# Kernel tuning notes

Measured on AMD Instinct MI355X. Metric: run time of the kernel, lower is better.

## Reference

```python
import jax, jax.numpy as jnp
import numpy as np

B, S, D, H, F = 16, 512, 768, 12, 3072
E = 4      # unique sequence-level experts
M = 4      # inner SwitchFeedForward experts
SW = 128   # switch encoder dim
EPS = 1e-12


def setup_inputs() -> dict:
    key = jax.random.key(0)
    ks = iter(jax.random.split(key, 64))
    def p(shape):
        return jax.random.normal(next(ks), shape, jnp.float32) * 0.02
    inp = {}
    inp['hidden_states'] = jax.random.normal(next(ks), (B, S, D), jnp.float32)
    inp['attention_mask'] = jnp.zeros((B, S), jnp.float32)
    inp['cluster_list'] = jnp.zeros((B,), jnp.int32)
    # router
    inp['sw_enc_w'] = p((D, SW)); inp['sw_enc_b'] = jnp.zeros((SW,), jnp.float32)
    inp['sw_w'] = p((SW, E));     inp['sw_b'] = jnp.zeros((E,), jnp.float32)
    # common attention
    for n in ('q', 'k', 'v', 'o'):
        inp['ca_w' + n] = p((D, D)); inp['ca_b' + n] = jnp.zeros((D,), jnp.float32)
    # unique attentions (stacked over E experts)
    for n in ('q', 'k', 'v', 'o'):
        inp['ua_w' + n] = p((E, D, D)); inp['ua_b' + n] = jnp.zeros((E, D), jnp.float32)
    # common FFN (plain GELU MLP)
    inp['cf_w1'] = p((D, F)); inp['cf_b1'] = jnp.zeros((F,), jnp.float32)
    inp['cf_w2'] = p((F, D)); inp['cf_b2'] = jnp.zeros((D,), jnp.float32)
    # unique FFNs: each is a top-1 SwitchFeedForward with M inner experts
    inp['uf_sw_w'] = p((E, D, M)); inp['uf_sw_b'] = jnp.zeros((E, M), jnp.float32)
    inp['uf_w1'] = p((E, M, D, F)); inp['uf_b1'] = jnp.zeros((E, M, F), jnp.float32)
    inp['uf_w2'] = p((E, M, F, D)); inp['uf_b2'] = jnp.zeros((E, M, D), jnp.float32)
    # output LayerNorm
    inp['ln_g'] = jnp.ones((D,), jnp.float32); inp['ln_b'] = jnp.zeros((D,), jnp.float32)
    return inp


def _attn(x, mask, wq, bq, wk, bk, wv, bv, wo, bo):
    b, s, d = x.shape
    dh = d // H
    q = (x @ wq + bq).reshape(b, s, H, dh)
    k = (x @ wk + bk).reshape(b, s, H, dh)
    v = (x @ wv + bv).reshape(b, s, H, dh)
    sc = jnp.einsum('bqhd,bkhd->bhqk', q, k) / jnp.sqrt(jnp.float32(dh))
    sc = sc + mask[:, None, None, :]
    pr = jax.nn.softmax(sc, axis=-1)
    o = jnp.einsum('bhqk,bkhd->bqhd', pr, v).reshape(b, s, d)
    return o @ wo + bo


def _switch_ffn(x, sww, swb, w1, b1, w2, b2):
    # top-1 token routing over M inner experts, output scaled by route_prob_max
    rp = jax.nn.softmax(x @ sww + swb, axis=-1)            # [b,s,M]
    gate = jax.nn.one_hot(jnp.argmax(rp, -1), M) * jnp.max(rp, -1, keepdims=True)
    h = jax.nn.gelu(jnp.einsum('bsd,mdf->bsmf', x, w1) + b1, approximate=False)
    y = jnp.einsum('bsmf,mfd->bsmd', h, w2) + b2
    return jnp.einsum('bsm,bsmd->bsd', gate, y)


def _forward(hidden_states, attention_mask, sw_enc_w, sw_enc_b, sw_w, sw_b,
             ca_wq, ca_bq, ca_wk, ca_bk, ca_wv, ca_bv, ca_wo, ca_bo,
             ua_wq, ua_bq, ua_wk, ua_bk, ua_wv, ua_bv, ua_wo, ua_bo,
             cf_w1, cf_b1, cf_w2, cf_b2,
             uf_sw_w, uf_sw_b, uf_w1, uf_b1, uf_w2, uf_b2, ln_g, ln_b):
    # sequence-level router: softmax over pooled hidden states, top-1 expert
    pooled = hidden_states.mean(axis=1)                    # [B,D]
    rp = jax.nn.softmax((pooled @ sw_enc_w + sw_enc_b) @ sw_w + sw_b, axis=-1)
    pm = jnp.max(rp, axis=-1)                              # [B]
    sel = jax.nn.one_hot(jnp.argmax(rp, axis=-1), E)       # [B,E]

    common_attn = _attn(hidden_states, attention_mask,
                        ca_wq, ca_bq, ca_wk, ca_bk, ca_wv, ca_bv, ca_wo, ca_bo)
    unique_attn = jnp.zeros_like(hidden_states)
    for i in range(E):
        oi = _attn(hidden_states, attention_mask,
                   ua_wq[i], ua_bq[i], ua_wk[i], ua_bk[i],
                   ua_wv[i], ua_bv[i], ua_wo[i], ua_bo[i])
        unique_attn = unique_attn + sel[:, i, None, None] * oi
    unique_attn = unique_attn * pm[:, None, None]          # scale by route prob
    att_output = common_attn + unique_attn

    unique_ffn = jnp.zeros_like(hidden_states)
    for i in range(E):
        yi = _switch_ffn(att_output, uf_sw_w[i], uf_sw_b[i],
                         uf_w1[i], uf_b1[i], uf_w2[i], uf_b2[i])
        unique_ffn = unique_ffn + sel[:, i, None, None] * yi
    common_ffn = jax.nn.gelu(att_output @ cf_w1 + cf_b1, approximate=False) @ cf_w2 + cf_b2
    ffn_output = common_ffn + unique_ffn                   # dropout is identity (eval)

    x = att_output + ffn_output
    mu = x.mean(-1, keepdims=True)
    var = jnp.mean((x - mu) ** 2, -1, keepdims=True)
    return (x - mu) / jnp.sqrt(var + EPS) * ln_g + ln_b


def reference(hidden_states, attention_mask, cluster_list, sw_enc_w, sw_enc_b, sw_w, sw_b,
              ca_wq, ca_bq, ca_wk, ca_bk, ca_wv, ca_bv, ca_wo, ca_bo,
              ua_wq, ua_bq, ua_wk, ua_bk, ua_wv, ua_bv, ua_wo, ua_bo,
              cf_w1, cf_b1, cf_w2, cf_b2,
              uf_sw_w, uf_sw_b, uf_w1, uf_b1, uf_w2, uf_b2, ln_g, ln_b):
    # cluster_list is only used in the warm-up branch; warm_up_step=0 -> ignored
    return _forward(hidden_states, attention_mask, sw_enc_w, sw_enc_b, sw_w, sw_b,
                    ca_wq, ca_bq, ca_wk, ca_bk, ca_wv, ca_bv, ca_wo, ca_bo,
                    ua_wq, ua_bq, ua_wk, ua_bk, ua_wv, ua_bv, ua_wo, ua_bo,
                    cf_w1, cf_b1, cf_w2, cf_b2,
                    uf_sw_w, uf_sw_b, uf_w1, uf_b1, uf_w2, uf_b2, ln_g, ln_b)
```

## Files before the change

### kernel.cpp

```cpp
#include <hip/hip_runtime.h>
#include <cstdint>
#include <cstddef>

#define Bq  16
#define Sq  512
#define Dq  768
#define Hq  12
#define DHq 64
#define Fq  3072
#define SWq 128
#define NTq 8192

typedef float        f32x4  __attribute__((ext_vector_type(4)));
typedef float        f32x16 __attribute__((ext_vector_type(16)));
typedef unsigned int u32x4  __attribute__((ext_vector_type(4)));
typedef __bf16       bf16x8 __attribute__((ext_vector_type(8)));
typedef _Float16     f16x8  __attribute__((ext_vector_type(8)));
typedef _Float16     f16x4  __attribute__((ext_vector_type(4)));
typedef _Float16     f16x2  __attribute__((ext_vector_type(2)));
typedef int          i32x2  __attribute__((ext_vector_type(2)));

__device__ __forceinline__ unsigned short f2bf(float f){
  unsigned int u = __builtin_bit_cast(unsigned int, f);
  u = (u + 0x7fffu + ((u >> 16) & 1u)) >> 16;
  return (unsigned short)u;
}
__device__ __forceinline__ unsigned int pk2(float a, float b){
  return (unsigned int)f2bf(a) | ((unsigned int)f2bf(b) << 16);
}
__device__ __forceinline__ i32x2 pl32swap(unsigned int a, unsigned int b){
  return __builtin_amdgcn_permlane32_swap((int)a, (int)b, false, false);
}
__device__ __forceinline__ f16x2 cvt_pk(float a, float b){
  return __builtin_bit_cast(f16x2, __builtin_amdgcn_cvt_pkrtz(a, b));
}

__device__ __forceinline__ void swz2d(int &bx, int &by){
  const int gx = gridDim.x, gy = gridDim.y;
  const int nb = gx * gy;
  const int bid = blockIdx.y * gx + blockIdx.x;
  if (((nb & 7) == 0) && ((gy & 7) == 0)){
    const int chunk = nb >> 3;
    const int lb = (bid & 7) * chunk + (bid >> 3);
    const int bw = gx << 3;
    const int band = lb / bw;
    const int wn = lb - band * bw;
    bx = wn >> 3;
    by = (band << 3) + (wn & 7);
  } else {
    bx = blockIdx.x; by = blockIdx.y;
  }
}

__global__ void pooled_partial_k(const float* __restrict__ x, float* __restrict__ part){
  const int b = blockIdx.x, dc = blockIdx.y, z = blockIdx.z;
  const int d = dc*256 + threadIdx.x;
  const float* p = x + (size_t)b*Sq*Dq + (size_t)z*128*Dq + d;
  float s = 0.f;
  #pragma unroll 4
  for (int i = 0; i < 128; i++) s += p[(size_t)i*Dq];
  part[((size_t)z*Bq + b)*Dq + d] = s;
}

__global__ void router_seq_k(const float* __restrict__ part,
    const float* __restrict__ ew, const float* __restrict__ eb,
    const float* __restrict__ sw, const float* __restrict__ sb,
    int* __restrict__ sel, float* __restrict__ pm)
{
  const int b = blockIdx.x, j = threadIdx.x;
  __shared__ float h[SWq];
  __shared__ float pl[Dq];
  #pragma unroll
  for (int i = 0; i < 6; i++){
    int d = j + i*128;
    float s = part[(size_t)(0*Bq+b)*Dq + d] + part[(size_t)(1*Bq+b)*Dq + d]
            + part[(size_t)(2*Bq+b)*Dq + d] + part[(size_t)(3*Bq+b)*Dq + d];
    pl[d] = s * (1.0f/512.0f);
  }
  __syncthreads();
  float a = eb[j];
  for (int d = 0; d < Dq; d++) a += pl[d] * ew[d*SWq + j];
  h[j] = a;
  __syncthreads();
  if (j == 0){
    float lg[4];
    for (int e = 0; e < 4; e++){
      float t = sb[e];
      for (int k = 0; k < SWq; k++) t += h[k] * sw[k*4 + e];
      lg[e] = t;
    }
    float mx = fmaxf(fmaxf(lg[0],lg[1]), fmaxf(lg[2],lg[3]));
    float p[4], ssum = 0.f;
    for (int e = 0; e < 4; e++){ p[e] = expf(lg[e]-mx); ssum += p[e]; }
    int am = 0; float bv = p[0];
    for (int e = 1; e < 4; e++) if (p[e] > bv){ bv = p[e]; am = e; }
    sel[b] = am; pm[b] = bv/ssum;
  }
}

__global__ void split_f16_k(const float* __restrict__ x, _Float16* __restrict__ hh,
                            _Float16* __restrict__ ll, int n4){
  const int i = blockIdx.x*256 + threadIdx.x;
  if (i >= n4) return;
  f32x4 v = ((const f32x4*)x)[i];
  f16x4 vh, vl;
  #pragma unroll
  for (int j = 0; j < 4; j++){
    float s = v[j] * 1024.0f;
    _Float16 a = (_Float16)s;
    vh[j] = a;
    vl[j] = (_Float16)(s - (float)a);
  }
  ((f16x4*)hh)[i] = vh;
  ((f16x4*)ll)[i] = vl;
}

__global__ void transpose_f16s_k(const float* __restrict__ src,
    _Float16* __restrict__ dH, _Float16* __restrict__ dL,
    int K, int N, long srcStride, long dstStride, int rowOff)
{
  __shared__ float t[64][65];
  const int tid = threadIdx.x;
  const size_t so = (size_t)blockIdx.z * srcStride;
  const size_t dof = (size_t)blockIdx.z * dstStride;
  const int k0 = blockIdx.y * 64, n0 = blockIdx.x * 64;
  const int r = tid >> 2, c0 = (tid & 3) * 16;
  const float* sp = src + so + (size_t)(k0 + r) * N + n0 + c0;
  #pragma unroll
  for (int cc = 0; cc < 16; cc += 4){
    f32x4 v = *(const f32x4*)(sp + cc);
    t[r][c0+cc] = v[0]; t[r][c0+cc+1] = v[1]; t[r][c0+cc+2] = v[2]; t[r][c0+cc+3] = v[3];
  }
  __syncthreads();
  _Float16* ph = dH + dof + (size_t)(rowOff + n0 + r) * K + k0 + c0;
  _Float16* pl = dL + dof + (size_t)(rowOff + n0 + r) * K + k0 + c0;
  #pragma unroll
  for (int cc = 0; cc < 16; cc += 4){
    f16x4 vh, vl;
    #pragma unroll
    for (int j = 0; j < 4; j++){
      float s = t[c0+cc+j][r] * 1024.0f;
      _Float16 a = (_Float16)s;
      vh[j] = a; vl[j] = (_Float16)(s - (float)a);
    }
    *(f16x4*)(ph + cc) = vh;
    *(f16x4*)(pl + cc) = vl;
  }
}

__global__ void concat_bias3_k(const float* __restrict__ bq, const float* __restrict__ bk,
    const float* __restrict__ bv, float* __restrict__ dst, int srcStride)
{
  const int e = blockIdx.y;
  const int i = blockIdx.x*256 + threadIdx.x;
  dst[(size_t)e*2304 + i]        = bq[(size_t)e*srcStride + i];
  dst[(size_t)e*2304 + 768 + i]  = bk[(size_t)e*srcStride + i];
  dst[(size_t)e*2304 + 1536 + i] = bv[(size_t)e*srcStride + i];
}

template<int BMODE, int OMODE>
__global__ __launch_bounds__(256,2) void gemm_f16s_k(
    const _Float16* __restrict__ AH, const _Float16* __restrict__ AL,
    const _Float16* __restrict__ BH, const _Float16* __restrict__ BL,
    const float* __restrict__ bias, float* __restrict__ C,
    _Float16* __restrict__ Ch, _Float16* __restrict__ Cl,
    int N, int K, long estride, int bias_stride,
    const int* __restrict__ sel, const float* __restrict__ pm)
{
  __shared__ _Float16 AsH[128][40];
  __shared__ _Float16 AsL[128][40];
  __shared__ _Float16 BsH[128][40];
  __shared__ _Float16 BsL[128][40];
  const int tid = threadIdx.x;
  const int lane = tid & 63, wave = tid >> 6;
  const int wm = wave >> 1, wn = wave & 1;
  int bx, by; swz2d(bx, by);
  const int row0 = by * 128, col0 = bx * 128;
  const _Float16* bh = BH; const _Float16* bl = BL; const float* bp = bias;
  float cs = 1.0f;
  if constexpr (BMODE == 1){
    const int e = sel[row0 >> 9];
    bh += (size_t)e * estride; bl += (size_t)e * estride;
    bp += (size_t)e * bias_stride;
  }
  if constexpr (OMODE == 1) cs = pm[row0 >> 9];

  const int sr = tid >> 1, sk = (tid & 1) * 16;
  const _Float16* ahp = AH + (size_t)(row0 + sr) * K + sk;
  const _Float16* alp = AL + (size_t)(row0 + sr) * K + sk;
  const _Float16* bhp = bh + (size_t)(col0 + sr) * K + sk;
  const _Float16* blp = bl + (size_t)(col0 + sr) * K + sk;

  f32x4 acc[4][4];
  #pragma unroll
  for (int mi=0;mi<4;mi++)
    #pragma unroll
    for (int ni=0;ni<4;ni++) acc[mi][ni] = (f32x4){0.f,0.f,0.f,0.f};

  for (int k0 = 0; k0 < K; k0 += 32){
    u32x4 vah0 = *(const u32x4*)(ahp + k0);
    u32x4 vah1 = *(const u32x4*)(ahp + k0 + 8);
    u32x4 val0 = *(const u32x4*)(alp + k0);
    u32x4 val1 = *(const u32x4*)(alp + k0 + 8);
    u32x4 vbh0 = *(const u32x4*)(bhp + k0);
    u32x4 vbh1 = *(const u32x4*)(bhp + k0 + 8);
    u32x4 vbl0 = *(const u32x4*)(blp + k0);
    u32x4 vbl1 = *(const u32x4*)(blp + k0 + 8);
    __syncthreads();
    *(u32x4*)&AsH[sr][sk]   = vah0; *(u32x4*)&AsH[sr][sk+8] = vah1;
    *(u32x4*)&AsL[sr][sk]   = val0; *(u32x4*)&AsL[sr][sk+8] = val1;
    *(u32x4*)&BsH[sr][sk]   = vbh0; *(u32x4*)&BsH[sr][sk+8] = vbh1;
    *(u32x4*)&BsL[sr][sk]   = vbl0; *(u32x4*)&BsL[sr][sk+8] = vbl1;
    __syncthreads();
    f16x8 fah[4], fal[4], fbh[4], fbl[4];
    #pragma unroll
    for (int mi=0;mi<4;mi++){
      const int r = wm*64 + mi*16 + (lane&15), c = 8*(lane>>4);
      fah[mi] = __builtin_bit_cast(f16x8, *(const u32x4*)&AsH[r][c]);
      fal[mi] = __builtin_bit_cast(f16x8, *(const u32x4*)&AsL[r][c]);
    }
    #pragma unroll
    for (int ni=0;ni<4;ni++){
      const int r = wn*64 + ni*16 + (lane&15), c = 8*(lane>>4);
      fbh[ni] = __builtin_bit_cast(f16x8, *(const u32x4*)&BsH[r][c]);
      fbl[ni] = __builtin_bit_cast(f16x8, *(const u32x4*)&BsL[r][c]);
    }
    #pragma unroll
    for (int mi=0;mi<4;mi++)
      #pragma unroll
      for (int ni=0;ni<4;ni++){
        acc[mi][ni] = __builtin_amdgcn_mfma_f32_16x16x32_f16(fah[mi], fbh[ni], acc[mi][ni], 0, 0, 0);
        acc[mi][ni] = __builtin_amdgcn_mfma_f32_16x16x32_f16(fah[mi], fbl[ni], acc[mi][ni], 0, 0, 0);
        acc[mi][ni] = __builtin_amdgcn_mfma_f32_16x16x32_f16(fal[mi], fbh[ni], acc[mi][ni], 0, 0, 0);
      }
  }

  const float INV = 1.0f/1048576.0f;
  const int erow = 4*(lane >> 4);
  const int ecol = lane & 15;
  #pragma unroll
  for (int mi=0;mi<4;mi++)
    #pragma unroll
    for (int ni=0;ni<4;ni++){
      const int c = col0 + wn*64 + ni*16 + ecol;
      const float bb = bp[c];
      #pragma unroll
      for (int r=0;r<4;r++){
        const int R = row0 + wm*64 + mi*16 + erow + r;
        const float v = acc[mi][ni][r]*INV + bb;
        if constexpr (OMODE == 0){
          C[(size_t)R*N + c] = v;
        } else if constexpr (OMODE == 1){
          C[(size_t)R*N + c] += cs*v;
        } else {
          const float vs = v * 1024.0f;
          const _Float16 hi = (_Float16)vs;
          Ch[(size_t)R*N + c] = hi;
          Cl[(size_t)R*N + c] = (_Float16)(vs - (float)hi);
        }
      }
    }
}

__global__ __launch_bounds__(256,2) void attn_mfma_k(
    const _Float16* __restrict__ qkvH, const _Float16* __restrict__ qkvL,
    const float* __restrict__ mask,
    _Float16* __restrict__ ctxH, _Float16* __restrict__ ctxL)
{
  __shared__ _Float16 Kh[64][72], Kl[64][72];
  __shared__ _Float16 Vh[64][72], Vl[64][72];
  __shared__ float msk[64];
  __shared__ float rsi[4][32];
  const int qb = blockIdx.x, h = blockIdx.y, b = blockIdx.z;
  const int tid = threadIdx.x;
  const int l = tid & 63, w = tid >> 6;
  const int l31 = l & 31, g5 = l >> 5;
  const float SC = 1.0f/8388608.0f;

  u32x4 qfh[4], qfl[4];
  {
    const size_t qoff = (size_t)(b*Sq + qb*128 + w*32 + l31) * 2304 + h*DHq + g5*8;
    #pragma unroll
    for (int c = 0; c < 4; c++){
      qfh[c] = *(const u32x4*)(qkvH + qoff + c*16);
      qfl[c] = *(const u32x4*)(qkvL + qoff + c*16);
    }
  }
  f32x16 oacc[2];
  #pragma unroll
  for (int nt = 0; nt < 2; nt++)
    #pragma unroll
    for (int i = 0; i < 16; i++) oacc[nt][i] = 0.f;
  float rsl = 0.f;
  const float* mrow = mask + b*Sq;

  for (int kt = 0; kt < 8; kt++){
    __syncthreads();
    {
      const size_t krow = (size_t)(b*Sq + kt*64 + l) * 2304 + 768 + h*DHq;
      #pragma unroll
      for (int i = 0; i < 2; i++){
        const int ch = w + i*4;
        *(u32x4*)&Kh[l][ch*8] = *(const u32x4*)(qkvH + krow + ch*8);
        *(u32x4*)&Kl[l][ch*8] = *(const u32x4*)(qkvL + krow + ch*8);
      }
      const size_t vrow = krow + 768 + w*16;
      f16x8 v0 = __builtin_bit_cast(f16x8, *(const u32x4*)(qkvH + vrow));
      f16x8 v1 = __builtin_bit_cast(f16x8, *(const u32x4*)(qkvH + vrow + 8));
      f16x8 u0 = __builtin_bit_cast(f16x8, *(const u32x4*)(qkvL + vrow));
      f16x8 u1 = __builtin_bit_cast(f16x8, *(const u32x4*)(qkvL + vrow + 8));
      #pragma unroll
      for (int i = 0; i < 8; i++){
        Vh[w*16 + i][l] = v0[i]; Vh[w*16 + 8 + i][l] = v1[i];
        Vl[w*16 + i][l] = u0[i]; Vl[w*16 + 8 + i][l] = u1[i];
      }
      if (tid < 64) msk[tid] = mrow[kt*64 + tid] + 6.9314718055994531f;
    }
    __syncthreads();

    f32x16 sacc[2];
    #pragma unroll
    for (int mt = 0; mt < 2; mt++)
      #pragma unroll
      for (int i = 0; i < 16; i++) sacc[mt][i] = 0.f;
    #pragma unroll
    for (int mt = 0; mt < 2; mt++){
      #pragma unroll
      for (int c = 0; c < 4; c++){
        f16x8 kh = __builtin_bit_cast(f16x8, *(const u32x4*)&Kh[mt*32 + l31][c*16 + g5*8]);
        f16x8 kl = __builtin_bit_cast(f16x8, *(const u32x4*)&Kl[mt*32 + l31][c*16 + g5*8]);
        f16x8 qh = __builtin_bit_cast(f16x8, qfh[c]);
        f16x8 ql = __builtin_bit_cast(f16x8, qfl[c]);
        sacc[mt] = __builtin_amdgcn_mfma_f32_32x32x16_f16(kh, qh, sacc[mt], 0, 0, 0);
        sacc[mt] = __builtin_amdgcn_mfma_f32_32x32x16_f16(kh, ql, sacc[mt], 0, 0, 0);
        sacc[mt] = __builtin_amdgcn_mfma_f32_32x32x16_f16(kl, qh, sacc[mt], 0, 0, 0);
      }
    }

    unsigned int hP[2][4][2], lP[2][4][2];
    #pragma unroll
    for (int mt = 0; mt < 2; mt++){
      #pragma unroll
      for (int m = 0; m < 4; m++){
        f32x4 mk = *(const f32x4*)&msk[mt*32 + m*8 + g5*4];
        float p0 = __expf(fmaf(sacc[mt][4*m+0], SC, mk[0]));
        float p1 = __expf(fmaf(sacc[mt][4*m+1], SC, mk[1]));
        float p2 = __expf(fmaf(sacc[mt][4*m+2], SC, mk[2]));
        float p3 = __expf(fmaf(sacc[mt][4*m+3], SC, mk[3]));
        rsl += (p0 + p1) + (p2 + p3);
        f16x2 h0 = cvt_pk(p0, p1);
        f16x2 h1 = cvt_pk(p2, p3);
        f16x2 e0, e1;
        e0[0] = (_Float16)(p0 - (float)h0[0]); e0[1] = (_Float16)(p1 - (float)h0[1]);
        e1[0] = (_Float16)(p2 - (float)h1[0]); e1[1] = (_Float16)(p3 - (float)h1[1]);
        hP[mt][m][0] = __builtin_bit_cast(unsigned int, h0);
        hP[mt][m][1] = __builtin_bit_cast(unsigned int, h1);
        lP[mt][m][0] = __builtin_bit_cast(unsigned int, e0);
        lP[mt][m][1] = __builtin_bit_cast(unsigned int, e1);
      }
    }

    #pragma unroll
    for (int mt = 0; mt < 2; mt++){
      #pragma unroll
      for (int cc = 0; cc < 2; cc++){
        i32x2 sh0 = pl32swap(hP[mt][2*cc][0], hP[mt][2*cc+1][0]);
        i32x2 sh1 = pl32swap(hP[mt][2*cc][1], hP[mt][2*cc+1][1]);
        i32x2 sl0 = pl32swap(lP[mt][2*cc][0], lP[mt][2*cc+1][0]);
        i32x2 sl1 = pl32swap(lP[mt][2*cc][1], lP[mt][2*cc+1][1]);
        u32x4 pah = (u32x4){(unsigned)sh0[0], (unsigned)sh1[0], (unsigned)sh0[1], (unsigned)sh1[1]};
        u32x4 pal = (u32x4){(unsigned)sl0[0], (unsigned)sl1[0], (unsigned)sl0[1], (unsigned)sl1[1]};
        f16x8 ph = __builtin_bit_cast(f16x8, pah);
        f16x8 pe = __builtin_bit_cast(f16x8, pal);
        const int kof = (mt*2 + cc)*16 + g5*8;
        #pragma unroll
        for (int nt = 0; nt < 2; nt++){
          f16x8 vh = __builtin_bit_cast(f16x8, *(const u32x4*)&Vh[nt*32 + l31][kof]);
          f16x8 vl = __builtin_bit_cast(f16x8, *(const u32x4*)&Vl[nt*32 + l31][kof]);
          oacc[nt] = __builtin_amdgcn_mfma_f32_32x32x16_f16(ph, vh, oacc[nt], 0, 0, 0);
          oacc[nt] = __builtin_amdgcn_mfma_f32_32x32x16_f16(ph, vl, oacc[nt], 0, 0, 0);
          oacc[nt] = __builtin_amdgcn_mfma_f32_32x32x16_f16(pe, vh, oacc[nt], 0, 0, 0);
        }
      }
    }
  }

  {
    unsigned int rb = __builtin_bit_cast(unsigned int, rsl);
    i32x2 sw = pl32swap(rb, rb);
    float partner = __builtin_bit_cast(float, (l >= 32) ? sw[0] : sw[1]);
    float tot = rsl + partner;
    if (l < 32) rsi[w][l31] = 1.0f / tot;
  }
  __syncthreads();

  const size_t obase = (size_t)(b*Sq + qb*128 + w*32);
  #pragma unroll
  for (int nt = 0; nt < 2; nt++){
    const int col = h*DHq + nt*32 + l31;
    #pragma unroll
    for (int r = 0; r < 16; r++){
      const int q = (r&3) + 8*(r>>2) + 4*g5;
      const float v = oacc[nt][r] * rsi[w][q];
      const _Float16 hi = (_Float16)v;
      const size_t off = (obase + q)*Dq + col;
      ctxH[off] = hi;
      ctxL[off] = (_Float16)(v - (float)hi);
    }
  }
}

__global__ void transpose_bf16_k(const float* __restrict__ src, unsigned short* __restrict__ dst,
                                 int K, int N)
{
  __shared__ float t[64][65];
  const int tid = threadIdx.x;
  const size_t mo = (size_t)blockIdx.z * K * N;
  const int k0 = blockIdx.y * 64, n0 = blockIdx.x * 64;
  const int r = tid >> 2, c0 = (tid & 3) * 16;
  const float* sp = src + mo + (size_t)(k0 + r) * N + n0 + c0;
  #pragma unroll
  for (int cc = 0; cc < 16; cc += 4){
    f32x4 v = *(const f32x4*)(sp + cc);
    t[r][c0+cc] = v[0]; t[r][c0+cc+1] = v[1]; t[r][c0+cc+2] = v[2]; t[r][c0+cc+3] = v[3];
  }
  __syncthreads();
  unsigned short* dp = dst + mo + (size_t)(n0 + r) * K + k0 + c0;
  u32x4 h0, h1v;
  #pragma unroll
  for (int i = 0; i < 4; i++) h0[i]  = pk2(t[c0+2*i  ][r], t[c0+2*i+1][r]);
  #pragma unroll
  for (int i = 0; i < 4; i++) h1v[i] = pk2(t[c0+8+2*i][r], t[c0+9+2*i][r]);
  *(u32x4*)(dp)     = h0;
  *(u32x4*)(dp + 8) = h1v;
}

template<int AMODE, int OMODE, bool GELU_, bool GROUPED>
__global__ __launch_bounds__(256,2) void gemm_bf16_k(
    const void* __restrict__ Av, const unsigned short* __restrict__ BT,
    const float* __restrict__ bias, float* __restrict__ Cf, unsigned short* __restrict__ Cb,
    int M, int N, int K,
    const int* __restrict__ tile_g, const int* __restrict__ tile_r0,
    const int* __restrict__ grp_off, const int* __restrict__ n_tiles,
    const int* __restrict__ tok_idx, const float* __restrict__ gate_s,
    size_t bstride, int bias_stride)
{
  __shared__ unsigned short As[128][40];
  __shared__ unsigned short Bs[128][40];
  const int tid = threadIdx.x;
  const int lane = tid & 63, wave = tid >> 6;
  const int wm = wave >> 1, wn = wave & 1;
  int col0, row0, gend = 1 << 30, g = 0;
  if constexpr (GROUPED){
    const int t = blockIdx.y;
    if (t >= *n_tiles) return;
    g = tile_g[t];
    row0 = grp_off[g] + tile_r0[t];
    gend = grp_off[g+1];
    col0 = blockIdx.x * 128;
  } else {
    int bx, by; swz2d(bx, by);
    row0 = by * 128;
    col0 = bx * 128;
  }
  const unsigned short* Bp = BT + (size_t)g * bstride;
  const float* bp = bias + (size_t)g * bias_stride;

  const int sr = tid >> 1;
  const int sk = (tid & 1) * 16;
  int arow = row0 + sr;
  if constexpr (GROUPED) arow = (arow < gend - 1) ? arow : (gend - 1);
  if constexpr (AMODE == 1) arow = tok_idx[arow];
  const float*          afp = (const float*)Av          + (size_t)arow * K + sk;
  const unsigned short* abp = (const unsigned short*)Av + (size_t)arow * K + sk;
  const unsigned short* bfp = Bp + (size_t)(col0 + sr) * K + sk;

  f32x4 acc[4][4];
  #pragma unroll
  for (int mi=0;mi<4;mi++)
    #pragma unroll
    for (int ni=0;ni<4;ni++) acc[mi][ni] = (f32x4){0.f,0.f,0.f,0.f};

  for (int k0 = 0; k0 < K; k0 += 32){
    u32x4 bl0 = *(const u32x4*)(bfp + k0);
    u32x4 bl1 = *(const u32x4*)(bfp + k0 + 8);
    u32x4 al0, al1;
    if constexpr (AMODE == 2){
      al0 = *(const u32x4*)(abp + k0);
      al1 = *(const u32x4*)(abp + k0 + 8);
    } else {
      f32x4 f0 = *(const f32x4*)(afp + k0);
      f32x4 f1 = *(const f32x4*)(afp + k0 + 4);
      f32x4 f2 = *(const f32x4*)(afp + k0 + 8);
      f32x4 f3 = *(const f32x4*)(afp + k0 + 12);
      al0[0]=pk2(f0[0],f0[1]); al0[1]=pk2(f0[2],f0[3]); al0[2]=pk2(f1[0],f1[1]); al0[3]=pk2(f1[2],f1[3]);
      al1[0]=pk2(f2[0],f2[1]); al1[1]=pk2(f2[2],f2[3]); al1[2]=pk2(f3[0],f3[1]); al1[3]=pk2(f3[2],f3[3]);
    }
    __syncthreads();
    *(u32x4*)&As[sr][sk]     = al0;
    *(u32x4*)&As[sr][sk + 8] = al1;
    *(u32x4*)&Bs[sr][sk]     = bl0;
    *(u32x4*)&Bs[sr][sk + 8] = bl1;
    __syncthreads();
    bf16x8 af[4], bfr[4];
    #pragma unroll
    for (int mi=0;mi<4;mi++){
      u32x4 t = *(const u32x4*)&As[wm*64 + mi*16 + (lane&15)][8*(lane>>4)];
      af[mi] = __builtin_bit_cast(bf16x8, t);
    }
    #pragma unroll
    for (int ni=0;ni<4;ni++){
      u32x4 t = *(const u32x4*)&Bs[wn*64 + ni*16 + (lane&15)][8*(lane>>4)];
      bfr[ni] = __builtin_bit_cast(bf16x8, t);
    }
    #pragma unroll
    for (int mi=0;mi<4;mi++)
      #pragma unroll
      for (int ni=0;ni<4;ni++)
        acc[mi][ni] = __builtin_amdgcn_mfma_f32_16x16x32_bf16(af[mi], bfr[ni], acc[mi][ni], 0, 0, 0);
  }

  const int erow = 4*(lane >> 4);
  const int ecol = lane & 15;
  #pragma unroll
  for (int mi=0;mi<4;mi++)
    #pragma unroll
    for (int ni=0;ni<4;ni++){
      const int c = col0 + wn*64 + ni*16 + ecol;
      const float bb = bp[c];
      #pragma unroll
      for (int r=0;r<4;r++){
        const int R = row0 + wm*64 + mi*16 + erow + r;
        if (GROUPED && R >= gend) continue;
        float v = acc[mi][ni][r] + bb;
        if (GELU_) v = 0.5f*v*(1.0f + erff(v*0.70710678118654752f));
        if constexpr (OMODE == 0){
          Cb[(size_t)R*N + c] = f2bf(v);
        } else if constexpr (OMODE == 1){
          Cf[(size_t)R*N + c] = v;
        } else {
          const int tok = tok_idx[R];
          const float gt = gate_s[R];
          float* p = Cf + (size_t)tok*N + c;
          *p += gt*v;
        }
      }
    }
}

__global__ void token_router_k(const float* __restrict__ att, const int* __restrict__ sel,
    const float* __restrict__ sww, const float* __restrict__ swb,
    int* __restrict__ grp, float* __restrict__ gate, int* __restrict__ grp_cnt)
{
  const int t = blockIdx.x*4 + (threadIdx.x >> 6);
  const int lane = threadIdx.x & 63;
  const int e = sel[t >> 9];
  const float* x = att + (size_t)t * Dq;
  const float* w = sww + (size_t)e * Dq * 4;
  float a0=0.f, a1=0.f, a2=0.f, a3=0.f;
  #pragma unroll 4
  for (int i = 0; i < 12; i++){
    const int d = lane + i*64;
    const float xv = x[d];
    f32x4 wv = *(const f32x4*)&w[d*4];
    a0 += xv*wv[0]; a1 += xv*wv[1]; a2 += xv*wv[2]; a3 += xv*wv[3];
  }
  #pragma unroll
  for (int off = 32; off; off >>= 1){
    a0 += __shfl_xor(a0, off); a1 += __shfl_xor(a1, off);
    a2 += __shfl_xor(a2, off); a3 += __shfl_xor(a3, off);
  }
  if (lane == 0){
    const float l0 = a0 + swb[e*4+0], l1 = a1 + swb[e*4+1];
    const float l2 = a2 + swb[e*4+2], l3 = a3 + swb[e*4+3];
    const float mx = fmaxf(fmaxf(l0,l1), fmaxf(l2,l3));
    const float p0 = expf(l0-mx), p1 = expf(l1-mx), p2 = expf(l2-mx), p3 = expf(l3-mx);
    const float ssum = p0+p1+p2+p3;
    int am = 0; float bv = p0;
    if (p1 > bv){ bv=p1; am=1; }
    if (p2 > bv){ bv=p2; am=2; }
    if (p3 > bv){ bv=p3; am=3; }
    grp[t] = e*4 + am;
    gate[t] = bv/ssum;
    atomicAdd(&grp_cnt[e*4 + am], 1);
  }
}

__global__ void build_offsets_k(const int* __restrict__ grp_cnt, int* __restrict__ grp_off,
    int* __restrict__ tile_g, int* __restrict__ tile_r0, int* __restrict__ n_tiles)
{
  int off = 0, nt = 0;
  for (int g = 0; g < 16; g++){
    grp_off[g] = off;
    const int c = grp_cnt[g];
    for (int r0 = 0; r0 < c; r0 += 128){ tile_g[nt] = g; tile_r0[nt] = r0; nt++; }
    off += c;
  }
  grp_off[16] = off;
  *n_tiles = nt;
}

__global__ void scatter_k(const int* __restrict__ grp, const float* __restrict__ gate,
    const int* __restrict__ grp_off, int* __restrict__ fill,
    int* __restrict__ tok_idx, float* __restrict__ gate_s)
{
  const int t = blockIdx.x*256 + threadIdx.x;
  const int g = grp[t];
  const int pos = grp_off[g] + atomicAdd(&fill[g], 1);
  tok_idx[pos] = t;
  gate_s[pos] = gate[t];
}

__global__ __launch_bounds__(256) void final_ln_k(const float* __restrict__ att,
    const float* __restrict__ acc, const float* __restrict__ lg,
    const float* __restrict__ lb, float* __restrict__ out)
{
  const int row = blockIdx.x, tid = threadIdx.x;
  const float* a = att + (size_t)row * Dq;
  const float* c = acc + (size_t)row * Dq;
  float x[3];
  #pragma unroll
  for (int i = 0; i < 3; i++) x[i] = a[tid + 256*i] + c[tid + 256*i];
  __shared__ float red[256];
  red[tid] = x[0] + x[1] + x[2];
  __syncthreads();
  for (int st = 128; st; st >>= 1){
    if (tid < st) red[tid] += red[tid + st];
    __syncthreads();
  }
  const float mu = red[0] * (1.0f/768.0f);
  __syncthreads();
  const float d0 = x[0]-mu, d1 = x[1]-mu, d2 = x[2]-mu;
  red[tid] = d0*d0 + d1*d1 + d2*d2;
  __syncthreads();
  for (int st = 128; st; st >>= 1){
    if (tid < st) red[tid] += red[tid + st];
    __syncthreads();
  }
  const float inv = 1.0f/sqrtf(red[0]*(1.0f/768.0f) + 1e-12f);
  #pragma unroll
  for (int i = 0; i < 3; i++){
    const int col = tid + 256*i;
    out[(size_t)row*Dq + col] = (x[i]-mu)*inv*lg[col] + lb[col];
  }
}

extern "C" void kernel_launch(void* const* d_in, const int* in_sizes, int n_in,
                              void* d_out, int out_size, void* d_ws, size_t ws_size,
                              hipStream_t stream)
{
  (void)in_sizes; (void)n_in; (void)out_size; (void)ws_size;
  const float* hs    = (const float*)d_in[0];
  const float* amask = (const float*)d_in[1];
  const float* sw_enc_w = (const float*)d_in[3];
  const float* sw_enc_b = (const float*)d_in[4];
  const float* sw_w  = (const float*)d_in[5];
  const float* sw_b  = (const float*)d_in[6];
  const float* ca_wq = (const float*)d_in[7];
  const float* ca_bq = (const float*)d_in[8];
  const float* ca_wk = (const float*)d_in[9];
  const float* ca_bk = (const float*)d_in[10];
  const float* ca_wv = (const float*)d_in[11];
  const float* ca_bv = (const float*)d_in[12];
  const float* ca_wo = (const float*)d_in[13];
  const float* ca_bo = (const float*)d_in[14];
  const float* ua_wq = (const float*)d_in[15];
  const float* ua_bq = (const float*)d_in[16];
  const float* ua_wk = (const float*)d_in[17];
  const float* ua_bk = (const float*)d_in[18];
  const float* ua_wv = (const float*)d_in[19];
  const float* ua_bv = (const float*)d_in[20];
  const float* ua_wo = (const float*)d_in[21];
  const float* ua_bo = (const float*)d_in[22];
  const float* cf_w1 = (const float*)d_in[23];
  const float* cf_b1 = (const float*)d_in[24];
  const float* cf_w2 = (const float*)d_in[25];
  const float* cf_b2 = (const float*)d_in[26];
  const float* uf_sw_w = (const float*)d_in[27];
  const float* uf_sw_b = (const float*)d_in[28];
  const float* uf_w1 = (const float*)d_in[29];
  const float* uf_b1 = (const float*)d_in[30];
  const float* uf_w2 = (const float*)d_in[31];
  const float* uf_b2 = (const float*)d_in[32];
  const float* ln_g  = (const float*)d_in[33];
  const float* ln_b  = (const float*)d_in[34];
  float* out = (float*)d_out;

  char* W = (char*)d_ws;
  int*   sel     = (int*)(W + 0);
  float* pm      = (float*)(W + 64);
  int*   grp_cnt = (int*)(W + 128);
  int*   fill    = (int*)(W + 192);
  int*   ntile   = (int*)(W + 256);
  int*   grp_off = (int*)(W + 512);
  int*   tile_g  = (int*)(W + 1024);
  int*   tile_r  = (int*)(W + 2048);

  float* att  = (float*)(W + 4096);
  float* facc = (float*)(W + 25169920);
  const size_t X = 50335744;
  _Float16* hsH  = (_Float16*)(W + X);
  _Float16* hsL  = (_Float16*)(W + X + 12582912);
  _Float16* qkvH = (_Float16*)(W + X + 25165824);
  _Float16* qkvL = (_Float16*)(W + X + 62914560);
  _Float16* ctxH = (_Float16*)(W + X + 100663296);
  _Float16* ctxL = (_Float16*)(W + X + 113246208);
  _Float16* wqkv_cH = (_Float16*)(W + X + 125829120);
  _Float16* wqkv_cL = (_Float16*)(W + X + 129368064);
  _Float16* wqkv_uH = (_Float16*)(W + X + 132907008);
  _Float16* wqkv_uL = (_Float16*)(W + X + 147062784);
  _Float16* wo_cH   = (_Float16*)(W + X + 161218560);
  _Float16* wo_cL   = (_Float16*)(W + X + 162398208);
  _Float16* wo_uH   = (_Float16*)(W + X + 163577856);
  _Float16* wo_uL   = (_Float16*)(W + X + 168296448);
  float* qkvb_c = (float*)(W + X + 173015040);
  float* qkvb_u = (float*)(W + X + 173024256);
  float* partb  = (float*)(W + X + 173061120);

  unsigned short* w1T = (unsigned short*)(W + X);
  unsigned short* w2T = (unsigned short*)(W + X + 80216064);
  unsigned short* h1  = (unsigned short*)(W + X + 160432128);
  int*   grp     = (int*)(W + 261099520);
  float* gate    = (float*)(W + 261132288);
  int*   tok_idx = (int*)(W + 261165056);
  float* gate_s  = (float*)(W + 261197824);

  hipMemsetAsync(W, 0, 3072, stream);

  pooled_partial_k<<<dim3(Bq,3,4),256,0,stream>>>(hs, partb);
  router_seq_k<<<Bq,128,0,stream>>>(partb, sw_enc_w, sw_enc_b, sw_w, sw_b, sel, pm);

  split_f16_k<<<6144,256,0,stream>>>(hs, hsH, hsL, NTq*Dq/4);
  transpose_f16s_k<<<dim3(12,12,1),256,0,stream>>>(ca_wq, wqkv_cH, wqkv_cL, Dq, Dq, 0, 0, 0);
  transpose_f16s_k<<<dim3(12,12,1),256,0,stream>>>(ca_wk, wqkv_cH, wqkv_cL, Dq, Dq, 0, 0, 768);
  transpose_f16s_k<<<dim3(12,12,1),256,0,stream>>>(ca_wv, wqkv_cH, wqkv_cL, Dq, Dq, 0, 0, 1536);
  transpose_f16s_k<<<dim3(12,12,4),256,0,stream>>>(ua_wq, wqkv_uH, wqkv_uL, Dq, Dq, (long)Dq*Dq, (long)2304*768, 0);
  transpose_f16s_k<<<dim3(12,12,4),256,0,stream>>>(ua_wk, wqkv_uH, wqkv_uL, Dq, Dq, (long)Dq*Dq, (long)2304*768, 768);
  transpose_f16s_k<<<dim3(12,12,4),256,0,stream>>>(ua_wv, wqkv_uH, wqkv_uL, Dq, Dq, (long)Dq*Dq, (long)2304*768, 1536);
  transpose_f16s_k<<<dim3(12,12,1),256,0,stream>>>(ca_wo, wo_cH, wo_cL, Dq, Dq, 0, 0, 0);
  transpose_f16s_k<<<dim3(12,12,4),256,0,stream>>>(ua_wo, wo_uH, wo_uL, Dq, Dq, (long)Dq*Dq, (long)Dq*Dq, 0);
  concat_bias3_k<<<dim3(3,1),256,0,stream>>>(ca_bq, ca_bk, ca_bv, qkvb_c, 0);
  concat_bias3_k<<<dim3(3,4),256,0,stream>>>(ua_bq, ua_bk, ua_bv, qkvb_u, 768);

  gemm_f16s_k<0,2><<<dim3(18,64),256,0,stream>>>(hsH, hsL, wqkv_cH, wqkv_cL, qkvb_c,
      nullptr, qkvH, qkvL, 2304, Dq, 0, 0, nullptr, nullptr);
  attn_mfma_k<<<dim3(4,Hq,Bq),256,0,stream>>>(qkvH, qkvL, amask, ctxH, ctxL);
  gemm_f16s_k<0,0><<<dim3(6,64),256,0,stream>>>(ctxH, ctxL, wo_cH, wo_cL, ca_bo,
      att, nullptr, nullptr, Dq, Dq, 0, 0, nullptr, nullptr);

  gemm_f16s_k<1,2><<<dim3(18,64),256,0,stream>>>(hsH, hsL, wqkv_uH, wqkv_uL, qkvb_u,
      nullptr, qkvH, qkvL, 2304, Dq, (long)2304*768, 2304, sel, nullptr);
  attn_mfma_k<<<dim3(4,Hq,Bq),256,0,stream>>>(qkvH, qkvL, amask, ctxH, ctxL);
  gemm_f16s_k<1,1><<<dim3(6,64),256,0,stream>>>(ctxH, ctxL, wo_uH, wo_uL, ua_bo,
      att, nullptr, nullptr, Dq, Dq, (long)Dq*Dq, Dq, sel, pm);

  transpose_bf16_k<<<dim3(48,12,1), 256,0,stream>>>(cf_w1, w1T, Dq, Fq);
  transpose_bf16_k<<<dim3(48,12,16),256,0,stream>>>(uf_w1, w1T + 2359296, Dq, Fq);
  transpose_bf16_k<<<dim3(12,48,1), 256,0,stream>>>(cf_w2, w2T, Fq, Dq);
  transpose_bf16_k<<<dim3(12,48,16),256,0,stream>>>(uf_w2, w2T + 2359296, Fq, Dq);

  gemm_bf16_k<0,0,true,false><<<dim3(24,64),256,0,stream>>>((const void*)att, w1T, cf_b1, nullptr, h1,
      NTq, Fq, Dq, nullptr,nullptr,nullptr,nullptr,nullptr,nullptr, (size_t)0, 0);
  gemm_bf16_k<2,1,false,false><<<dim3(6,64),256,0,stream>>>((const void*)h1, w2T, cf_b2, facc, nullptr,
      NTq, Dq, Fq, nullptr,nullptr,nullptr,nullptr,nullptr,nullptr, (size_t)0, 0);

  token_router_k<<<2048,256,0,stream>>>(att, sel, uf_sw_w, uf_sw_b, grp, gate, grp_cnt);
  build_offsets_k<<<1,1,0,stream>>>(grp_cnt, grp_off, tile_g, tile_r, ntile);
  scatter_k<<<32,256,0,stream>>>(grp, gate, grp_off, fill, tok_idx, gate_s);

  gemm_bf16_k<1,0,true,true><<<dim3(24,80),256,0,stream>>>((const void*)att, w1T + 2359296, uf_b1, nullptr, h1,
      NTq, Fq, Dq, tile_g, tile_r, grp_off, ntile, tok_idx, gate_s, (size_t)2359296, Fq);
  gemm_bf16_k<2,2,false,true><<<dim3(6,80),256,0,stream>>>((const void*)h1, w2T + 2359296, uf_b2, facc, nullptr,
      NTq, Dq, Fq, tile_g, tile_r, grp_off, ntile, tok_idx, gate_s, (size_t)2359296, Dq);

  final_ln_k<<<NTq,256,0,stream>>>(att, facc, ln_g, ln_b, out);
}
```

Before: 1.224 ms.

## Use 64-row tiles for down-projection GEMMs and remap grouped tile order

Templates the bf16 GEMM on row-tile height and runs the two F->D down-projection GEMMs (common and grouped expert) with 64-row tiles. This doubles their block count so the small N=768 grids fill more compute units. The grouped kernel also remaps the linear block index with a stride-8 interleave, and build_offsets now emits both 128-row and 64-row tile lists. In exchange, each block reuses fewer B-tile loads per MFMA, and the shared-memory layout shifts.

```diff
diff --git a/kernel.cpp b/kernel.cpp
--- a/kernel.cpp
+++ b/kernel.cpp
@@ -435,49 +435,57 @@
   *(u32x4*)(dp + 8) = h1v;
 }
 
-template<int AMODE, int OMODE, bool GELU_, bool GROUPED>
+template<int MT, int AMODE, int OMODE, bool GELU_, bool GROUPED>
 __global__ __launch_bounds__(256,2) void gemm_bf16_k(
     const void* __restrict__ Av, const unsigned short* __restrict__ BT,
     const float* __restrict__ bias, float* __restrict__ Cf, unsigned short* __restrict__ Cb,
-    int M, int N, int K,
+    int N, int K,
     const int* __restrict__ tile_g, const int* __restrict__ tile_r0,
     const int* __restrict__ grp_off, const int* __restrict__ n_tiles,
     const int* __restrict__ tok_idx, const float* __restrict__ gate_s,
     size_t bstride, int bias_stride)
 {
-  __shared__ unsigned short As[128][40];
+  constexpr int MI = MT / 32;
+  __shared__ unsigned short As[MT][40];
   __shared__ unsigned short Bs[128][40];
   const int tid = threadIdx.x;
   const int lane = tid & 63, wave = tid >> 6;
   const int wm = wave >> 1, wn = wave & 1;
   int col0, row0, gend = 1 << 30, g = 0;
   if constexpr (GROUPED){
-    const int t = blockIdx.y;
+    const int gx = gridDim.x;
+    const int nb = gx * gridDim.y;
+    const int bid = blockIdx.y * gx + blockIdx.x;
+    int lb = bid;
+    if ((nb & 7) == 0) lb = (bid & 7) * (nb >> 3) + (bid >> 3);
+    const int t = lb / gx;
+    col0 = (lb - t * gx) * 128;
     if (t >= *n_tiles) return;
     g = tile_g[t];
     row0 = grp_off[g] + tile_r0[t];
     gend = grp_off[g+1];
-    col0 = blockIdx.x * 128;
   } else {
     int bx, by; swz2d(bx, by);
-    row0 = by * 128;
+    row0 = by * MT;
     col0 = bx * 128;
   }
   const unsigned short* Bp = BT + (size_t)g * bstride;
   const float* bp = bias + (size_t)g * bias_stride;
 
-  const int sr = tid >> 1;
-  const int sk = (tid & 1) * 16;
-  int arow = row0 + sr;
+  const int sa_r = (MT == 128) ? (tid >> 1) : (tid >> 2);
+  const int sa_k = (MT == 128) ? ((tid & 1) * 16) : ((tid & 3) * 8);
+  const int sb_r = tid >> 1;
+  const int sb_k = (tid & 1) * 16;
+  int arow = row0 + sa_r;
   if constexpr (GROUPED) arow = (arow < gend - 1) ? arow : (gend - 1);
   if constexpr (AMODE == 1) arow = tok_idx[arow];
-  const float*          afp = (const float*)Av          + (size_t)arow * K + sk;
-  const unsigned short* abp = (const unsigned short*)Av + (size_t)arow * K + sk;
-  const unsigned short* bfp = Bp + (size_t)(col0 + sr) * K + sk;
-
-  f32x4 acc[4][4];
-  #pragma unroll
-  for (int mi=0;mi<4;mi++)
+  const float*          afp = (const float*)Av          + (size_t)arow * K + sa_k;
+  const unsigned short* abp = (const unsigned short*)Av + (size_t)arow * K + sa_k;
+  const unsigned short* bfp = Bp + (size_t)(col0 + sb_r) * K + sb_k;
+
+  f32x4 acc[MI][4];
+  #pragma unroll
+  for (int mi=0;mi<MI;mi++)
     #pragma unroll
     for (int ni=0;ni<4;ni++) acc[mi][ni] = (f32x4){0.f,0.f,0.f,0.f};
 
@@ -487,25 +495,27 @@
     u32x4 al0, al1;
     if constexpr (AMODE == 2){
       al0 = *(const u32x4*)(abp + k0);
-      al1 = *(const u32x4*)(abp + k0 + 8);
+      if constexpr (MT == 128) al1 = *(const u32x4*)(abp + k0 + 8);
     } else {
       f32x4 f0 = *(const f32x4*)(afp + k0);
       f32x4 f1 = *(const f32x4*)(afp + k0 + 4);
-      f32x4 f2 = *(const f32x4*)(afp + k0 + 8);
-      f32x4 f3 = *(const f32x4*)(afp + k0 + 12);
       al0[0]=pk2(f0[0],f0[1]); al0[1]=pk2(f0[2],f0[3]); al0[2]=pk2(f1[0],f1[1]); al0[3]=pk2(f1[2],f1[3]);
-      al1[0]=pk2(f2[0],f2[1]); al1[1]=pk2(f2[2],f2[3]); al1[2]=pk2(f3[0],f3[1]); al1[3]=pk2(f3[2],f3[3]);
+      if constexpr (MT == 128){
+        f32x4 f2 = *(const f32x4*)(afp + k0 + 8);
+        f32x4 f3 = *(const f32x4*)(afp + k0 + 12);
+        al1[0]=pk2(f2[0],f2[1]); al1[1]=pk2(f2[2],f2[3]); al1[2]=pk2(f3[0],f3[1]); al1[3]=pk2(f3[2],f3[3]);
+      }
     }
     __syncthreads();
-    *(u32x4*)&As[sr][sk]     = al0;
-    *(u32x4*)&As[sr][sk + 8] = al1;
-    *(u32x4*)&Bs[sr][sk]     = bl0;
-    *(u32x4*)&Bs[sr][sk + 8] = bl1;
+    *(u32x4*)&As[sa_r][sa_k] = al0;
+    if constexpr (MT == 128) *(u32x4*)&As[sa_r][sa_k + 8] = al1;
+    *(u32x4*)&Bs[sb_r][sb_k]     = bl0;
+    *(u32x4*)&Bs[sb_r][sb_k + 8] = bl1;
     __syncthreads();
-    bf16x8 af[4], bfr[4];
-    #pragma unroll
-    for (int mi=0;mi<4;mi++){
-      u32x4 t = *(const u32x4*)&As[wm*64 + mi*16 + (lane&15)][8*(lane>>4)];
+    bf16x8 af[MI], bfr[4];
+    #pragma unroll
+    for (int mi=0;mi<MI;mi++){
+      u32x4 t = *(const u32x4*)&As[wm*(MT/2) + mi*16 + (lane&15)][8*(lane>>4)];
       af[mi] = __builtin_bit_cast(bf16x8, t);
     }
     #pragma unroll
@@ -514,7 +524,7 @@
       bfr[ni] = __builtin_bit_cast(bf16x8, t);
     }
     #pragma unroll
-    for (int mi=0;mi<4;mi++)
+    for (int mi=0;mi<MI;mi++)
       #pragma unroll
       for (int ni=0;ni<4;ni++)
         acc[mi][ni] = __builtin_amdgcn_mfma_f32_16x16x32_bf16(af[mi], bfr[ni], acc[mi][ni], 0, 0, 0);
@@ -523,14 +533,14 @@
   const int erow = 4*(lane >> 4);
   const int ecol = lane & 15;
   #pragma unroll
-  for (int mi=0;mi<4;mi++)
+  for (int mi=0;mi<MI;mi++)
     #pragma unroll
     for (int ni=0;ni<4;ni++){
       const int c = col0 + wn*64 + ni*16 + ecol;
       const float bb = bp[c];
       #pragma unroll
       for (int r=0;r<4;r++){
-        const int R = row0 + wm*64 + mi*16 + erow + r;
+        const int R = row0 + wm*(MT/2) + mi*16 + erow + r;
         if (GROUPED && R >= gend) continue;
         float v = acc[mi][ni][r] + bb;
         if (GELU_) v = 0.5f*v*(1.0f + erff(v*0.70710678118654752f));
@@ -587,17 +597,19 @@
 }
 
 __global__ void build_offsets_k(const int* __restrict__ grp_cnt, int* __restrict__ grp_off,
-    int* __restrict__ tile_g, int* __restrict__ tile_r0, int* __restrict__ n_tiles)
-{
-  int off = 0, nt = 0;
+    int* __restrict__ tg128, int* __restrict__ tr128, int* __restrict__ nt128,
+    int* __restrict__ tg64, int* __restrict__ tr64, int* __restrict__ nt64)
+{
+  int off = 0, n1 = 0, n2 = 0;
   for (int g = 0; g < 16; g++){
     grp_off[g] = off;
     const int c = grp_cnt[g];
-    for (int r0 = 0; r0 < c; r0 += 128){ tile_g[nt] = g; tile_r0[nt] = r0; nt++; }
+    for (int r0 = 0; r0 < c; r0 += 128){ tg128[n1] = g; tr128[n1] = r0; n1++; }
+    for (int r0 = 0; r0 < c; r0 += 64){  tg64[n2]  = g; tr64[n2]  = r0; n2++; }
     off += c;
   }
   grp_off[16] = off;
-  *n_tiles = nt;
+  *nt128 = n1; *nt64 = n2;
 }
 
 __global__ void scatter_k(const int* __restrict__ grp, const float* __restrict__ gate,
@@ -692,13 +704,16 @@
   int*   grp_cnt = (int*)(W + 128);
   int*   fill    = (int*)(W + 192);
   int*   ntile   = (int*)(W + 256);
+  int*   ntile64 = (int*)(W + 320);
   int*   grp_off = (int*)(W + 512);
   int*   tile_g  = (int*)(W + 1024);
   int*   tile_r  = (int*)(W + 2048);
-
-  float* att  = (float*)(W + 4096);
-  float* facc = (float*)(W + 25169920);
-  const size_t X = 50335744;
+  int*   tile_g64= (int*)(W + 3072);
+  int*   tile_r64= (int*)(W + 4096);
+
+  float* att  = (float*)(W + 8192);
+  float* facc = (float*)(W + 25174016);
+  const size_t X = 50339840;
   _Float16* hsH  = (_Float16*)(W + X);
   _Float16* hsL  = (_Float16*)(W + X + 12582912);
   _Float16* qkvH = (_Float16*)(W + X + 25165824);
@@ -720,12 +735,12 @@
   unsigned short* w1T = (unsigned short*)(W + X);
   unsigned short* w2T = (unsigned short*)(W + X + 80216064);
   unsigned short* h1  = (unsigned short*)(W + X + 160432128);
-  int*   grp     = (int*)(W + 261099520);
-  float* gate    = (float*)(W + 261132288);
-  int*   tok_idx = (int*)(W + 261165056);
-  float* gate_s  = (float*)(W + 261197824);
-
-  hipMemsetAsync(W, 0, 3072, stream);
+  int*   grp     = (int*)(W + 261103616);
+  float* gate    = (float*)(W + 261136384);
+  int*   tok_idx = (int*)(W + 261169152);
+  float* gate_s  = (float*)(W + 261201920);
+
+  hipMemsetAsync(W, 0, 512, stream);
 
   pooled_partial_k<<<dim3(Bq,3,4),256,0,stream>>>(hs, partb);
   router_seq_k<<<Bq,128,0,stream>>>(partb, sw_enc_w, sw_enc_b, sw_w, sw_b, sel, pm);
@@ -759,19 +774,19 @@
   transpose_bf16_k<<<dim3(12,48,1), 256,0,stream>>>(cf_w2, w2T, Fq, Dq);
   transpose_bf16_k<<<dim3(12,48,16),256,0,stream>>>(uf_w2, w2T + 2359296, Fq, Dq);
 
-  gemm_bf16_k<0,0,true,false><<<dim3(24,64),256,0,stream>>>((const void*)att, w1T, cf_b1, nullptr, h1,
-      NTq, Fq, Dq, nullptr,nullptr,nullptr,nullptr,nullptr,nullptr, (size_t)0, 0);
-  gemm_bf16_k<2,1,false,false><<<dim3(6,64),256,0,stream>>>((const void*)h1, w2T, cf_b2, facc, nullptr,
-      NTq, Dq, Fq, nullptr,nullptr,nullptr,nullptr,nullptr,nullptr, (size_t)0, 0);
+  gemm_bf16_k<128,0,0,true,false><<<dim3(24,64),256,0,stream>>>((const void*)att, w1T, cf_b1, nullptr, h1,
+      Fq, Dq, nullptr,nullptr,nullptr,nullptr,nullptr,nullptr, (size_t)0, 0);
+  gemm_bf16_k<64,2,1,false,false><<<dim3(6,128),256,0,stream>>>((const void*)h1, w2T, cf_b2, facc, nullptr,
+      Dq, Fq, nullptr,nullptr,nullptr,nullptr,nullptr,nullptr, (size_t)0, 0);
 
   token_router_k<<<2048,256,0,stream>>>(att, sel, uf_sw_w, uf_sw_b, grp, gate, grp_cnt);
-  build_offsets_k<<<1,1,0,stream>>>(grp_cnt, grp_off, tile_g, tile_r, ntile);
+  build_offsets_k<<<1,1,0,stream>>>(grp_cnt, grp_off, tile_g, tile_r, ntile, tile_g64, tile_r64, ntile64);
   scatter_k<<<32,256,0,stream>>>(grp, gate, grp_off, fill, tok_idx, gate_s);
 
-  gemm_bf16_k<1,0,true,true><<<dim3(24,80),256,0,stream>>>((const void*)att, w1T + 2359296, uf_b1, nullptr, h1,
-      NTq, Fq, Dq, tile_g, tile_r, grp_off, ntile, tok_idx, gate_s, (size_t)2359296, Fq);
-  gemm_bf16_k<2,2,false,true><<<dim3(6,80),256,0,stream>>>((const void*)h1, w2T + 2359296, uf_b2, facc, nullptr,
-      NTq, Dq, Fq, tile_g, tile_r, grp_off, ntile, tok_idx, gate_s, (size_t)2359296, Dq);
+  gemm_bf16_k<128,1,0,true,true><<<dim3(24,80),256,0,stream>>>((const void*)att, w1T + 2359296, uf_b1, nullptr, h1,
+      Fq, Dq, tile_g, tile_r, grp_off, ntile, tok_idx, gate_s, (size_t)2359296, Fq);
+  gemm_bf16_k<64,2,2,false,true><<<dim3(6,144),256,0,stream>>>((const void*)h1, w2T + 2359296, uf_b2, facc, nullptr,
+      Dq, Fq, tile_g64, tile_r64, grp_off, ntile64, tok_idx, gate_s, (size_t)2359296, Dq);
 
   final_ln_k<<<NTq,256,0,stream>>>(att, facc, ln_g, ln_b, out);
 }
```

New measurement: 1.217 ms. No clear change (-0.6%).
